# Optimization experiments

Measured on AMD Instinct MI355X. Metric: run time of the kernel, lower is better.

## Reference

```python
import jax, jax.numpy as jnp
import numpy as np

# dims: B batches, N points/batch, S sampled points/batch, M image-projected points/batch,
# V voxels, (H,Wd) range-image size, HID hidden size, NSC scales, NCLS classes
B, N, S, M, V, H, Wd, HID, NSC, NCLS = 2, 120000, 40000, 30000, 100000, 256, 1024, 128, 4, 20


def setup_inputs() -> dict:
    key = jax.random.key(0)
    ks = jax.random.split(key, 24)
    f = jnp.float32
    w = lambda k, shp: (0.02 * jax.random.normal(k, shp, f))
    rows = jax.random.randint(ks[10], (B, M), 0, H, jnp.int32)
    cols = jax.random.randint(ks[11], (B, M), 0, Wd, jnp.int32)
    return {
        "pts_feat_layers": jax.random.normal(ks[0], (NSC, V, HID), f),
        "pts_sample_feat": jax.random.normal(ks[1], (NSC, B * S, HID), f),
        "img_latent_full": jax.random.normal(ks[2], (B, HID, H, Wd), f),
        "img_feat_layers": jax.random.normal(ks[3], (NSC, B * M, HID), f),
        "leaner_W": w(ks[4], (NSC, HID, HID)), "leaner_b": jnp.zeros((NSC, HID), f),
        "fcs1_W": w(ks[5], (NSC, 2 * HID, HID)), "fcs1_b": jnp.zeros((NSC, HID), f),
        "fcs2_W": w(ks[6], (NSC, HID, HID)), "fcs2_b": jnp.zeros((NSC, HID), f),
        "cls_W1": w(ks[7], (NSC * HID, 128)), "cls_b1": jnp.zeros((128,), f),
        "cls_W2": w(ks[8], (128, NCLS)), "cls_b2": jnp.zeros((NCLS,), f),
        "points_img": jnp.stack([rows, cols], axis=-1),              # [B,M,2]
        "point2img_index": jax.random.randint(ks[12], (B, M), 0, N, jnp.int32),
        "sample_index": jax.random.randint(ks[13], (B, S), 0, N, jnp.int32),
        "coors_inv": jax.random.randint(ks[14], (B * N,), 0, V, jnp.int32),
    }


def reference(pts_feat_layers, pts_sample_feat, img_latent_full, img_feat_layers,
              leaner_W, leaner_b, fcs1_W, fcs1_b, fcs2_W, fcs2_b,
              cls_W1, cls_b1, cls_W2, cls_b2,
              points_img, point2img_index, sample_index, coors_inv):
    dt = img_latent_full.dtype
    img_hw = jnp.transpose(img_latent_full, (0, 2, 3, 1))  # [B,H,Wd,HID]
    bar = jnp.arange(B)[:, None]
    # gather image features at projected pixel coords: [B,M,HID]
    img_at_pts = img_hw[bar, points_img[:, :, 0], points_img[:, :, 1]]
    # scatter image features to per-point slots (pts_img_batch_new): [B,N,HID]
    pimg = jax.vmap(lambda idx, v: jnp.zeros((N, HID), dt).at[idx].set(v))(point2img_index, img_at_pts)

    fuse_feats, enc_feats = [], []
    for i in range(NSC):
        # p2img_mapping_spsample: output values depend only on sampled feats + image gather
        sf = pts_sample_feat[i].reshape(B, S, HID)
        sp = jax.vmap(lambda idx, v: jnp.zeros((N, HID), dt).at[idx].set(v))(sample_index, sf)
        sp = sp + pimg  # sample_point_feat == sample_point_feat_f  [B,N,HID]
        # scatter fused point features back into voxel features, then gather per point
        pts_feat = pts_feat_layers[i].at[coors_inv].set(sp.reshape(B * N, HID))
        pts_point = pts_feat[coors_inv].reshape(B, N, HID)
        # p2img_mapping: gather the image-projected points per batch  [B*M,HID]
        pts_g = jnp.take_along_axis(pts_point, point2img_index[:, :, None], axis=1).reshape(B * M, HID)
        fl = jax.nn.relu(pts_g @ leaner_W[i] + leaner_b[i])
        fc = jnp.concatenate([img_feat_layers[i], fl], axis=1) @ fcs1_W[i] + fcs1_b[i]
        fw = jax.nn.sigmoid(fc @ fcs2_W[i] + fcs2_b[i])
        fuse_feats.append(jax.nn.relu(fc * fw))
        enc_feats.append(sp.reshape(B * N, HID))

    seg = jnp.concatenate(fuse_feats, axis=1)                       # [B*M, NSC*HID]
    img_seg_logits = jax.nn.relu(seg @ cls_W1 + cls_b1) @ cls_W2 + cls_b2  # [B*M, NCLS]
    output_3d = jnp.concatenate(enc_feats, axis=1)                  # [B*N, NSC*HID]
    return img_seg_logits, output_3d
```

## Files before the change

kernel.cpp:

```cpp
#include <hip/hip_runtime.h>
#include <hip/hip_bf16.h>
#include <math.h>

#define B_    2
#define N_    120000
#define S_    40000
#define M_    30000
#define V_    100000
#define H_    256
#define WD_   1024
#define HID_  128
#define NSC_  4
#define NCLS_ 20
#define BM_   60000
#define BS_   80000
#define BN_   240000

typedef __attribute__((ext_vector_type(8))) short bfrag8;
typedef __attribute__((ext_vector_type(4))) float facc4;
typedef __attribute__((ext_vector_type(4))) unsigned short usvec4;

__device__ __forceinline__ unsigned short f2bf(float f){
  unsigned u = __builtin_bit_cast(unsigned, f);
  u += 0x7fffu + ((u >> 16) & 1u);
  return (unsigned short)(u >> 16);
}
__device__ __forceinline__ float bf2f(unsigned short s){
  return __builtin_bit_cast(float, ((unsigned)s) << 16);
}

__global__ __launch_bounds__(256) void k_front(
    const float* __restrict__ img, const int* __restrict__ ptsimg,
    unsigned short* __restrict__ iap,
    const int* __restrict__ p2i, const int* __restrict__ si,
    const int* __restrict__ ci,
    int* __restrict__ win_p, int* __restrict__ win_s, int* __restrict__ win_c,
    const float* __restrict__ lW, const float* __restrict__ f1W,
    const float* __restrict__ f2W, const float* __restrict__ c1W,
    const float* __restrict__ c2W,
    unsigned short* __restrict__ lwT, unsigned short* __restrict__ f1T,
    unsigned short* __restrict__ f2T, unsigned short* __restrict__ c1T,
    unsigned short* __restrict__ c2T){
  int bid = blockIdx.x;
  if (bid < 938){
    int t = bid * 256 + threadIdx.x;
    if (t < BM_) atomicMax(&win_p[(t / M_) * N_ + p2i[t]], t);
    if (t < BS_) atomicMax(&win_s[(t / S_) * N_ + si[t]], t);
    if (t < BN_) atomicMax(&win_c[ci[t]], t);
    return;
  }
  if (bid < 2228){
    int t = (bid - 938) * 256 + threadIdx.x;
    if (t < 65536){
      int i = t >> 14, r = t & 16383, n = r >> 7, k = r & 127;
      lwT[i * 16384 + n * 128 + k] = f2bf(lW[i * 16384 + k * 128 + n]);
    } else if (t < 196608){
      int e = t - 65536;
      int i = e >> 15, r = e & 32767, n = r >> 8, k = r & 255;
      f1T[i * 32768 + n * 256 + k] = f2bf(f1W[i * 32768 + k * 128 + n]);
    } else if (t < 262144){
      int e = t - 196608;
      int i = e >> 14, r = e & 16383, n = r >> 7, k = r & 127;
      f2T[i * 16384 + n * 128 + k] = f2bf(f2W[i * 16384 + k * 128 + n]);
    } else if (t < 327680){
      int e = t - 262144;
      int n = e >> 9, k = e & 511;
      c1T[n * 512 + k] = f2bf(c1W[k * 128 + n]);
    } else if (t < 330240){
      int e = t - 327680;
      int n = e >> 7, k = e & 127;
      c2T[n * 128 + k] = f2bf(c2W[k * NCLS_ + n]);
    }
    return;
  }
  {
    int t = (bid - 2228) * 256 + threadIdx.x;
    int r0 = t >> 5, h4 = (t & 31) * 4;
    const size_t st = (size_t)H_ * WD_;
    #pragma unroll
    for (int half = 0; half < 2; half++){
      int row = r0 + half * 30000;
      int r = ptsimg[row * 2 + 0];
      int c = ptsimg[row * 2 + 1];
      const float* base = img + (((size_t)half * HID_ + h4) * H_ + r) * WD_ + c;
      float v0 = base[0], v1 = base[st], v2 = base[2 * st], v3 = base[3 * st];
      usvec4 o = {f2bf(v0), f2bf(v1), f2bf(v2), f2bf(v3)};
      *(usvec4*)(iap + (size_t)row * HID_ + h4) = o;
    }
    return;
  }
}

__global__ __launch_bounds__(256) void k_o3d(const float* __restrict__ samp,
    const int* __restrict__ win_s, const int* __restrict__ win_p,
    const unsigned short* __restrict__ iap, float* __restrict__ o3d){
  const facc4 zero = {0.f, 0.f, 0.f, 0.f};
  int t = blockIdx.x * 256 + threadIdx.x;
  int jg = t >> 5, q = t & 31;
  int j0 = jg << 2;
  int sjv[4], pjv[4];
  #pragma unroll
  for (int jj = 0; jj < 4; jj++){ sjv[jj] = win_s[j0 + jj]; pjv[jj] = win_p[j0 + jj]; }
  facc4 iv[4];
  #pragma unroll
  for (int jj = 0; jj < 4; jj++){
    int p = pjv[jj] < 0 ? 0 : pjv[jj];
    usvec4 u = *(const usvec4*)(iap + (size_t)p * HID_ + q * 4);
    facc4 v = {bf2f(u.x), bf2f(u.y), bf2f(u.z), bf2f(u.w)};
    iv[jj] = pjv[jj] >= 0 ? v : zero;
  }
  #pragma unroll
  for (int i = 0; i < NSC_; i++){
    #pragma unroll
    for (int jj = 0; jj < 4; jj++){
      int s = sjv[jj] < 0 ? 0 : sjv[jj];
      facc4 sv = *(const facc4*)(samp + ((size_t)i * BS_ + s) * HID_ + q * 4);
      facc4 v = iv[jj] + (sjv[jj] >= 0 ? sv : zero);
      __builtin_nontemporal_store(v,
          (facc4*)(o3d + (size_t)(j0 + jj) * (NSC_ * HID_) + i * HID_ + q * 4));
    }
  }
}

__global__ __launch_bounds__(256, 3) void k_scales(
    const float* __restrict__ samp, const unsigned short* __restrict__ iap,
    const int* __restrict__ win_p, const int* __restrict__ win_s,
    const int* __restrict__ win_c, const int* __restrict__ p2i,
    const int* __restrict__ ci, const float* __restrict__ imgf,
    const unsigned short* __restrict__ lwT, const float* __restrict__ lb,
    const unsigned short* __restrict__ f1T, const float* __restrict__ f1b,
    const unsigned short* __restrict__ f2T, const float* __restrict__ f2b,
    unsigned short* __restrict__ seg){
  __shared__ char lds[49152];
  char* actL = lds + 32768;
  const int i  = blockIdx.x & 3;
  const int rb = blockIdx.x >> 2;
  const int lane = threadIdx.x & 63, wv = threadIdx.x >> 6;
  const int rl = lane & 15, kg = lane >> 4;
  const int rowBase = rb * 64 + wv * 16;
  const int row = rowBase + rl;
  const bool rv = row < BM_;
  const int lr = wv * 16 + rl;

  {
    const char* src = (const char*)(lwT + (size_t)i * 16384);
    for (int c = threadIdx.x; c < 2048; c += 256){
      int byte = c << 4; int n = byte >> 8;
      *(bfrag8*)(lds + (byte ^ ((n & 7) << 4))) = *(const bfrag8*)(src + byte);
    }
  }
  bfrag8 afr[4];
  {
    int g = 0;
    if (rv){ int b = row >= M_; g = win_c[ci[b * N_ + p2i[row]]]; }
    int sj = rv ? win_s[g] : -1;
    int pj = rv ? win_p[g] : -1;
    const float* sp = samp + ((size_t)i * BS_ + (sj < 0 ? 0 : sj)) * HID_;
    const unsigned short* pp = iap + (size_t)(pj < 0 ? 0 : pj) * HID_;
    #pragma unroll
    for (int kc = 0; kc < 4; kc++){
      int k0 = kc * 32 + kg * 8;
      facc4 s0 = {0,0,0,0}, s1 = {0,0,0,0};
      if (sj >= 0){ s0 = *(const facc4*)(sp + k0); s1 = *(const facc4*)(sp + k0 + 4); }
      float g0=0,g1=0,g2=0,g3=0,g4=0,g5=0,g6=0,g7=0;
      if (pj >= 0){
        usvec4 u0 = *(const usvec4*)(pp + k0);
        usvec4 u1 = *(const usvec4*)(pp + k0 + 4);
        g0=bf2f(u0.x); g1=bf2f(u0.y); g2=bf2f(u0.z); g3=bf2f(u0.w);
        g4=bf2f(u1.x); g5=bf2f(u1.y); g6=bf2f(u1.z); g7=bf2f(u1.w);
      }
      bfrag8 a;
      a[0]=(short)f2bf(s0.x+g0); a[1]=(short)f2bf(s0.y+g1);
      a[2]=(short)f2bf(s0.z+g2); a[3]=(short)f2bf(s0.w+g3);
      a[4]=(short)f2bf(s1.x+g4); a[5]=(short)f2bf(s1.y+g5);
      a[6]=(short)f2bf(s1.z+g6); a[7]=(short)f2bf(s1.w+g7);
      afr[kc] = a;
    }
  }
  __syncthreads();
  facc4 accL[8];
  #pragma unroll
  for (int ct = 0; ct < 8; ct++) accL[ct] = (facc4){0.f,0.f,0.f,0.f};
  #pragma unroll
  for (int kc = 0; kc < 4; kc++){
    int k0 = kc * 32 + kg * 8;
    #pragma unroll
    for (int ct = 0; ct < 8; ct++){
      int col = ct * 16 + rl;
      int byte = (col << 8) + (k0 << 1);
      bfrag8 b = *(const bfrag8*)(lds + (byte ^ ((col & 7) << 4)));
      accL[ct] = __builtin_amdgcn_mfma_f32_16x16x32_bf16(afr[kc], b, accL[ct], 0, 0, 0);
    }
  }
  __syncthreads();
  {
    const float* bias = lb + i * HID_;
    #pragma unroll
    for (int ct = 0; ct < 8; ct++){
      int col = ct * 16 + rl;
      float bv = bias[col];
      #pragma unroll
      for (int r = 0; r < 4; r++){
        int ar = wv * 16 + kg * 4 + r;
        float v = accL[ct][r] + bv; v = v > 0.f ? v : 0.f;
        int byte = ar * 256 + col * 2;
        *(unsigned short*)(actL + (byte ^ ((ar & 7) << 4))) = f2bf(v);
      }
    }
    const char* src = (const char*)(f1T + (size_t)i * 32768);
    for (int c = threadIdx.x; c < 2048; c += 256){
      int n = c >> 4, off = (c & 15) << 4;
      *(bfrag8*)(lds + ((n * 256 + off) ^ ((n & 7) << 4))) =
          *(const bfrag8*)(src + (size_t)n * 512 + off);
    }
  }
  __syncthreads();
  facc4 accF[8];
  #pragma unroll
  for (int ct = 0; ct < 8; ct++) accF[ct] = (facc4){0.f,0.f,0.f,0.f};
  {
    const float* a1 = imgf + ((size_t)i * BM_ + (rv ? row : 0)) * HID_;
    #pragma unroll
    for (int kc = 0; kc < 4; kc++){
      int kk = kc * 32 + kg * 8;
      bfrag8 a = (bfrag8){0,0,0,0,0,0,0,0};
      if (rv){
        facc4 s0 = *(const facc4*)(a1 + kk);
        facc4 s1 = *(const facc4*)(a1 + kk + 4);
        a[0]=(short)f2bf(s0.x); a[1]=(short)f2bf(s0.y); a[2]=(short)f2bf(s0.z); a[3]=(short)f2bf(s0.w);
        a[4]=(short)f2bf(s1.x); a[5]=(short)f2bf(s1.y); a[6]=(short)f2bf(s1.z); a[7]=(short)f2bf(s1.w);
      }
      #pragma unroll
      for (int ct = 0; ct < 8; ct++){
        int col = ct * 16 + rl;
        int byte = (col << 8) + (kk << 1);
        bfrag8 b = *(const bfrag8*)(lds + (byte ^ ((col & 7) << 4)));
        accF[ct] = __builtin_amdgcn_mfma_f32_16x16x32_bf16(a, b, accF[ct], 0, 0, 0);
      }
    }
  }
  __syncthreads();
  {
    const char* src = (const char*)(f1T + (size_t)i * 32768) + 256;
    for (int c = threadIdx.x; c < 2048; c += 256){
      int n = c >> 4, off = (c & 15) << 4;
      *(bfrag8*)(lds + ((n * 256 + off) ^ ((n & 7) << 4))) =
          *(const bfrag8*)(src + (size_t)n * 512 + off);
    }
  }
  __syncthreads();
  #pragma unroll
  for (int kc = 0; kc < 4; kc++){
    int kl = kc * 32 + kg * 8;
    int byteA = lr * 256 + kl * 2;
    bfrag8 a = *(const bfrag8*)(actL + (byteA ^ ((lr & 7) << 4)));
    #pragma unroll
    for (int ct = 0; ct < 8; ct++){
      int col = ct * 16 + rl;
      int byte = (col << 8) + (kl << 1);
      bfrag8 b = *(const bfrag8*)(lds + (byte ^ ((col & 7) << 4)));
      accF[ct] = __builtin_amdgcn_mfma_f32_16x16x32_bf16(a, b, accF[ct], 0, 0, 0);
    }
  }
  __syncthreads();
  {
    const float* bias = f1b + i * HID_;
    #pragma unroll
    for (int ct = 0; ct < 8; ct++){
      int col = ct * 16 + rl;
      float bv = bias[col];
      #pragma unroll
      for (int r = 0; r < 4; r++){
        int ar = wv * 16 + kg * 4 + r;
        float v = accF[ct][r] + bv;
        accF[ct][r] = v;
        int byte = ar * 256 + col * 2;
        *(unsigned short*)(actL + (byte ^ ((ar & 7) << 4))) = f2bf(v);
      }
    }
    const char* src = (const char*)(f2T + (size_t)i * 16384);
    for (int c = threadIdx.x; c < 2048; c += 256){
      int byte = c << 4; int n = byte >> 8;
      *(bfrag8*)(lds + (byte ^ ((n & 7) << 4))) = *(const bfrag8*)(src + byte);
    }
  }
  __syncthreads();
  facc4 accT[8];
  #pragma unroll
  for (int ct = 0; ct < 8; ct++) accT[ct] = (facc4){0.f,0.f,0.f,0.f};
  #pragma unroll
  for (int kc = 0; kc < 4; kc++){
    int kk = kc * 32 + kg * 8;
    int byteA = lr * 256 + kk * 2;
    bfrag8 a = *(const bfrag8*)(actL + (byteA ^ ((lr & 7) << 4)));
    #pragma unroll
    for (int ct = 0; ct < 8; ct++){
      int col = ct * 16 + rl;
      int byte = (col << 8) + (kk << 1);
      bfrag8 b = *(const bfrag8*)(lds + (byte ^ ((col & 7) << 4)));
      accT[ct] = __builtin_amdgcn_mfma_f32_16x16x32_bf16(a, b, accT[ct], 0, 0, 0);
    }
  }
  {
    const float* bias2 = f2b + i * HID_;
    #pragma unroll
    for (int ct = 0; ct < 8; ct++){
      int col = ct * 16 + rl;
      float bv2 = bias2[col];
      #pragma unroll
      for (int r = 0; r < 4; r++){
        int orow = rowBase + kg * 4 + r;
        if (orow < BM_){
          float tv = accT[ct][r] + bv2;
          float fw = 1.f / (1.f + expf(-tv));
          float u = accF[ct][r] * fw;
          u = u > 0.f ? u : 0.f;
          seg[(size_t)orow * (NSC_ * HID_) + i * HID_ + col] = f2bf(u);
        }
      }
    }
  }
}

__global__ __launch_bounds__(256, 3) void k_cls(const unsigned short* __restrict__ seg,
    const unsigned short* __restrict__ c1T, const float* __restrict__ c1b,
    const unsigned short* __restrict__ c2T, const float* __restrict__ c2b,
    float* __restrict__ logits){
  __shared__ char lds[49152];
  char* actL = lds + 32768;
  const int lane = threadIdx.x & 63, wv = threadIdx.x >> 6;
  const int rl = lane & 15, kg = lane >> 4;
  const int rowBase = blockIdx.x * 64 + wv * 16;
  const int row = rowBase + rl;
  const bool rv = row < BM_;
  const unsigned short* ar = seg + (size_t)(rv ? row : 0) * 512;
  facc4 acc[8];
  #pragma unroll
  for (int ct = 0; ct < 8; ct++) acc[ct] = (facc4){0.f,0.f,0.f,0.f};
  for (int ph = 0; ph < 4; ph++){
    if (ph) __syncthreads();
    for (int c = threadIdx.x; c < 2048; c += 256){
      int n = c >> 4, off = (c & 15) << 4;
      *(bfrag8*)(lds + ((n * 256 + off) ^ ((n & 7) << 4))) =
          *(const bfrag8*)((const char*)c1T + (size_t)n * 1024 + ph * 256 + off);
    }
    __syncthreads();
    #pragma unroll
    for (int kc = 0; kc < 4; kc++){
      int kl = kc * 32 + kg * 8;
      bfrag8 a = (bfrag8){0,0,0,0,0,0,0,0};
      if (rv) a = *(const bfrag8*)(ar + ph * 128 + kl);
      #pragma unroll
      for (int ct = 0; ct < 8; ct++){
        int col = ct * 16 + rl;
        int byte = (col << 8) + (kl << 1);
        bfrag8 b = *(const bfrag8*)(lds + (byte ^ ((col & 7) << 4)));
        acc[ct] = __builtin_amdgcn_mfma_f32_16x16x32_bf16(a, b, acc[ct], 0, 0, 0);
      }
    }
  }
  __syncthreads();
  #pragma unroll
  for (int ct = 0; ct < 8; ct++){
    int col = ct * 16 + rl;
    float bv = c1b[col];
    #pragma unroll
    for (int r = 0; r < 4; r++){
      int arr = wv * 16 + kg * 4 + r;
      float v = acc[ct][r] + bv; v = v > 0.f ? v : 0.f;
      int byte = arr * 256 + col * 2;
      *(unsigned short*)(actL + (byte ^ ((arr & 7) << 4))) = f2bf(v);
    }
  }
  for (int c = threadIdx.x; c < 320; c += 256)
    *(bfrag8*)(lds + (c << 4)) = *(const bfrag8*)((const char*)c2T + (c << 4));
  __syncthreads();
  {
    int t = threadIdx.x;
    int lrd = t >> 2, n0 = (t & 3) * 5;
    int orow = blockIdx.x * 64 + lrd;
    if (orow < BM_){
      float accD[5];
      #pragma unroll
      for (int q = 0; q < 5; q++) accD[q] = c2b[n0 + q];
      #pragma unroll
      for (int k8 = 0; k8 < 16; k8++){
        int byteA = lrd * 256 + (k8 << 4);
        bfrag8 hv = *(const bfrag8*)(actL + (byteA ^ ((lrd & 7) << 4)));
        #pragma unroll
        for (int q = 0; q < 5; q++){
          bfrag8 w8 = *(const bfrag8*)(lds + (n0 + q) * 256 + (k8 << 4));
          #pragma unroll
          for (int e = 0; e < 8; e++)
            accD[q] += bf2f((unsigned short)hv[e]) * bf2f((unsigned short)w8[e]);
        }
      }
      #pragma unroll
      for (int q = 0; q < 5; q++)
        logits[(size_t)orow * NCLS_ + n0 + q] = accD[q];
    }
  }
}

extern "C" void kernel_launch(void* const* d_in, const int* in_sizes, int n_in,
                              void* d_out, int out_size, void* d_ws, size_t ws_size,
                              hipStream_t stream){
  const float* samp = (const float*)d_in[1];
  const float* img  = (const float*)d_in[2];
  const float* imgf = (const float*)d_in[3];
  const float* lW   = (const float*)d_in[4];
  const float* lb   = (const float*)d_in[5];
  const float* f1W  = (const float*)d_in[6];
  const float* f1b  = (const float*)d_in[7];
  const float* f2W  = (const float*)d_in[8];
  const float* f2b  = (const float*)d_in[9];
  const float* c1W  = (const float*)d_in[10];
  const float* c1b  = (const float*)d_in[11];
  const float* c2W  = (const float*)d_in[12];
  const float* c2b  = (const float*)d_in[13];
  const int* ptsimg = (const int*)d_in[14];
  const int* p2i    = (const int*)d_in[15];
  const int* si     = (const int*)d_in[16];
  const int* ci     = (const int*)d_in[17];

  char* ws = (char*)d_ws;
  int*   win_p = (int*)(ws + 0);
  int*   win_s = (int*)(ws + 960000);
  int*   win_c = (int*)(ws + 1920000);
  unsigned short* iap = (unsigned short*)(ws + 2320128);
  unsigned short* seg = (unsigned short*)(ws + 17680384);
  unsigned short* lwT = (unsigned short*)(ws + 79120512);
  unsigned short* f1T = lwT + 65536;
  unsigned short* f2T = f1T + 131072;
  unsigned short* c1T = f2T + 65536;
  unsigned short* c2T = c1T + 65536;

  float* logits = (float*)d_out;
  float* o3d    = (float*)d_out + (size_t)BM_ * NCLS_;

  (void)hipMemsetAsync(ws, 0xFF, 2320000, stream);
  k_front  <<<5978,  256, 0, stream>>>(img, ptsimg, iap, p2i, si, ci,
                                       win_p, win_s, win_c,
                                       lW, f1W, f2W, c1W, c2W,
                                       lwT, f1T, f2T, c1T, c2T);
  k_o3d    <<<7500,  256, 0, stream>>>(samp, win_s, win_p, iap, o3d);
  k_scales <<<3752,  256, 0, stream>>>(samp, iap, win_p, win_s, win_c, p2i, ci,
                                       imgf, lwT, lb, f1T, f1b, f2T, f2b, seg);
  k_cls    <<<938,   256, 0, stream>>>(seg, c1T, c1b, c2T, c2b, logits);
}
```

Baseline: 466.1 us.

## Enlarge k_scales blocks to 128 rows and widen per-thread image gather

k_scales now runs 512-thread blocks covering 128 rows with 64KB of LDS. Each staged weight tile is therefore reused across twice as many rows, which cuts global weight reads and staging passes per row. The image-feature gather in k_front now assigns 4 threads per row, each reading 32 channel values and writing 16-byte bf16 stores, so the grid shrinks. The larger LDS footprint and block size may lower occupancy, and the gather has fewer threads in flight to hide strided-load latency.

```diff
diff --git a/kernel.cpp b/kernel.cpp
--- a/kernel.cpp
+++ b/kernel.cpp
@@ -75,17 +75,24 @@
   }
   {
     int t = (bid - 2228) * 256 + threadIdx.x;
-    int r0 = t >> 5, h4 = (t & 31) * 4;
+    int row = t >> 2;
+    if (row >= BM_) return;
+    int h0 = (t & 3) * 32;
+    int b = row >= M_;
+    int r = ptsimg[row * 2 + 0];
+    int c = ptsimg[row * 2 + 1];
+    const float* base = img + (((size_t)b * HID_ + h0) * H_ + r) * WD_ + c;
     const size_t st = (size_t)H_ * WD_;
-    #pragma unroll
-    for (int half = 0; half < 2; half++){
-      int row = r0 + half * 30000;
-      int r = ptsimg[row * 2 + 0];
-      int c = ptsimg[row * 2 + 1];
-      const float* base = img + (((size_t)half * HID_ + h4) * H_ + r) * WD_ + c;
-      float v0 = base[0], v1 = base[st], v2 = base[2 * st], v3 = base[3 * st];
-      usvec4 o = {f2bf(v0), f2bf(v1), f2bf(v2), f2bf(v3)};
-      *(usvec4*)(iap + (size_t)row * HID_ + h4) = o;
+    unsigned short* dst = iap + (size_t)row * HID_ + h0;
+    #pragma unroll
+    for (int g = 0; g < 4; g++){
+      float v[8];
+      #pragma unroll
+      for (int e = 0; e < 8; e++) v[e] = base[(size_t)(g * 8 + e) * st];
+      bfrag8 o;
+      #pragma unroll
+      for (int e = 0; e < 8; e++) o[e] = (short)f2bf(v[e]);
+      *(bfrag8*)(dst + g * 8) = o;
     }
     return;
   }
@@ -122,7 +129,7 @@
   }
 }
 
-__global__ __launch_bounds__(256, 3) void k_scales(
+__global__ __launch_bounds__(512, 4) void k_scales(
     const float* __restrict__ samp, const unsigned short* __restrict__ iap,
     const int* __restrict__ win_p, const int* __restrict__ win_s,
     const int* __restrict__ win_c, const int* __restrict__ p2i,
@@ -131,20 +138,21 @@
     const unsigned short* __restrict__ f1T, const float* __restrict__ f1b,
     const unsigned short* __restrict__ f2T, const float* __restrict__ f2b,
     unsigned short* __restrict__ seg){
-  __shared__ char lds[49152];
+  __shared__ char lds[65536];
   char* actL = lds + 32768;
   const int i  = blockIdx.x & 3;
   const int rb = blockIdx.x >> 2;
-  const int lane = threadIdx.x & 63, wv = threadIdx.x >> 6;
+  const int tid = threadIdx.x;
+  const int lane = tid & 63, wv = tid >> 6;
   const int rl = lane & 15, kg = lane >> 4;
-  const int rowBase = rb * 64 + wv * 16;
+  const int rowBase = rb * 128 + wv * 16;
   const int row = rowBase + rl;
   const bool rv = row < BM_;
   const int lr = wv * 16 + rl;
 
   {
     const char* src = (const char*)(lwT + (size_t)i * 16384);
-    for (int c = threadIdx.x; c < 2048; c += 256){
+    for (int c = tid; c < 2048; c += 512){
       int byte = c << 4; int n = byte >> 8;
       *(bfrag8*)(lds + (byte ^ ((n & 7) << 4))) = *(const bfrag8*)(src + byte);
     }
@@ -208,7 +216,7 @@
       }
     }
     const char* src = (const char*)(f1T + (size_t)i * 32768);
-    for (int c = threadIdx.x; c < 2048; c += 256){
+    for (int c = tid; c < 2048; c += 512){
       int n = c >> 4, off = (c & 15) << 4;
       *(bfrag8*)(lds + ((n * 256 + off) ^ ((n & 7) << 4))) =
           *(const bfrag8*)(src + (size_t)n * 512 + off);
@@ -242,7 +250,7 @@
   __syncthreads();
   {
     const char* src = (const char*)(f1T + (size_t)i * 32768) + 256;
-    for (int c = threadIdx.x; c < 2048; c += 256){
+    for (int c = tid; c < 2048; c += 512){
       int n = c >> 4, off = (c & 15) << 4;
       *(bfrag8*)(lds + ((n * 256 + off) ^ ((n & 7) << 4))) =
           *(const bfrag8*)(src + (size_t)n * 512 + off);
@@ -279,7 +287,7 @@
       }
     }
     const char* src = (const char*)(f2T + (size_t)i * 16384);
-    for (int c = threadIdx.x; c < 2048; c += 256){
+    for (int c = tid; c < 2048; c += 512){
       int byte = c << 4; int n = byte >> 8;
       *(bfrag8*)(lds + (byte ^ ((n & 7) << 4))) = *(const bfrag8*)(src + byte);
     }
@@ -439,12 +447,12 @@
   float* o3d    = (float*)d_out + (size_t)BM_ * NCLS_;
 
   (void)hipMemsetAsync(ws, 0xFF, 2320000, stream);
-  k_front  <<<5978,  256, 0, stream>>>(img, ptsimg, iap, p2i, si, ci,
+  k_front  <<<3166,  256, 0, stream>>>(img, ptsimg, iap, p2i, si, ci,
                                        win_p, win_s, win_c,
                                        lW, f1W, f2W, c1W, c2W,
                                        lwT, f1T, f2T, c1T, c2T);
   k_o3d    <<<7500,  256, 0, stream>>>(samp, win_s, win_p, iap, o3d);
-  k_scales <<<3752,  256, 0, stream>>>(samp, iap, win_p, win_s, win_c, p2i, ci,
+  k_scales <<<1876,  512, 0, stream>>>(samp, iap, win_p, win_s, win_c, p2i, ci,
                                        imgf, lwT, lb, f1T, f1b, f2T, f2b, seg);
   k_cls    <<<938,   256, 0, stream>>>(seg, c1T, c1b, c2T, c2b, logits);
 }
```

New measurement: 481.2 us. 1.03x slower.

## Split fused per-scale MLP kernel into three persistent-tile GEMM kernels

Applied to the files above, without the earlier changes.

Breaks the single k_scales kernel, which ran leaner, fcs1 and fcs2 back to back with LDS weight reloads and many barriers, into three kernels: k_leaner, k_fcs1 and k_fcs2g. Each block now loads its weight tile into LDS once and reuses it across four 64-row tiles, and fcs1/fcs2 split the output columns in halves to shrink LDS per block. The cost is extra global round-trips for bf16 intermediates (fl and fc, about 15 MB each) and two more kernel launches. Occupancy is also raised to 4 blocks per CU.

```diff
diff --git a/kernel.cpp b/kernel.cpp
--- a/kernel.cpp
+++ b/kernel.cpp
@@ -122,44 +122,51 @@
   }
 }
 
-__global__ __launch_bounds__(256, 3) void k_scales(
+__global__ __launch_bounds__(256, 4) void k_leaner(
     const float* __restrict__ samp, const unsigned short* __restrict__ iap,
     const int* __restrict__ win_p, const int* __restrict__ win_s,
     const int* __restrict__ win_c, const int* __restrict__ p2i,
-    const int* __restrict__ ci, const float* __restrict__ imgf,
+    const int* __restrict__ ci,
     const unsigned short* __restrict__ lwT, const float* __restrict__ lb,
-    const unsigned short* __restrict__ f1T, const float* __restrict__ f1b,
-    const unsigned short* __restrict__ f2T, const float* __restrict__ f2b,
-    unsigned short* __restrict__ seg){
-  __shared__ char lds[49152];
-  char* actL = lds + 32768;
-  const int i  = blockIdx.x & 3;
-  const int rb = blockIdx.x >> 2;
-  const int lane = threadIdx.x & 63, wv = threadIdx.x >> 6;
-  const int rl = lane & 15, kg = lane >> 4;
-  const int rowBase = rb * 64 + wv * 16;
-  const int row = rowBase + rl;
-  const bool rv = row < BM_;
-  const int lr = wv * 16 + rl;
-
+    unsigned short* __restrict__ fl){
+  __shared__ char lds[32768];
+  const int i = blockIdx.x & 3, bis = blockIdx.x >> 2;
+  const int tid = threadIdx.x;
+  const int lane = tid & 63, wv = tid >> 6;
+  const int rl = lane & 15, kg = lane >> 4, kgo = kg * 8;
   {
     const char* src = (const char*)(lwT + (size_t)i * 16384);
-    for (int c = threadIdx.x; c < 2048; c += 256){
+    for (int c = tid; c < 2048; c += 256){
       int byte = c << 4; int n = byte >> 8;
       *(bfrag8*)(lds + (byte ^ ((n & 7) << 4))) = *(const bfrag8*)(src + byte);
     }
   }
-  bfrag8 afr[4];
-  {
-    int g = 0;
-    if (rv){ int b = row >= M_; g = win_c[ci[b * N_ + p2i[row]]]; }
-    int sj = rv ? win_s[g] : -1;
-    int pj = rv ? win_p[g] : -1;
+  int sjv[4], pjv[4];
+  #pragma unroll
+  for (int t = 0; t < 4; t++){
+    int row = (bis * 4 + t) * 64 + wv * 16 + rl;
+    int sj = -1, pj = -1;
+    if (row < BM_){
+      int b = row >= M_;
+      int g = win_c[ci[b * N_ + p2i[row]]];
+      sj = win_s[g]; pj = win_p[g];
+    }
+    sjv[t] = sj; pjv[t] = pj;
+  }
+  __syncthreads();
+  float bv[8];
+  #pragma unroll
+  for (int ct = 0; ct < 8; ct++) bv[ct] = lb[i * HID_ + ct * 16 + rl];
+  #pragma unroll 1
+  for (int t = 0; t < 4; t++){
+    int rowBase = (bis * 4 + t) * 64 + wv * 16;
+    int sj = sjv[t], pj = pjv[t];
     const float* sp = samp + ((size_t)i * BS_ + (sj < 0 ? 0 : sj)) * HID_;
     const unsigned short* pp = iap + (size_t)(pj < 0 ? 0 : pj) * HID_;
+    bfrag8 afr[4];
     #pragma unroll
     for (int kc = 0; kc < 4; kc++){
-      int k0 = kc * 32 + kg * 8;
+      int k0 = kc * 32 + kgo;
       facc4 s0 = {0,0,0,0}, s1 = {0,0,0,0};
       if (sj >= 0){ s0 = *(const facc4*)(sp + k0); s1 = *(const facc4*)(sp + k0 + 4); }
       float g0=0,g1=0,g2=0,g3=0,g4=0,g5=0,g6=0,g7=0;
@@ -176,144 +183,154 @@
       a[6]=(short)f2bf(s1.z+g6); a[7]=(short)f2bf(s1.w+g7);
       afr[kc] = a;
     }
-  }
-  __syncthreads();
-  facc4 accL[8];
-  #pragma unroll
-  for (int ct = 0; ct < 8; ct++) accL[ct] = (facc4){0.f,0.f,0.f,0.f};
-  #pragma unroll
-  for (int kc = 0; kc < 4; kc++){
-    int k0 = kc * 32 + kg * 8;
-    #pragma unroll
-    for (int ct = 0; ct < 8; ct++){
-      int col = ct * 16 + rl;
-      int byte = (col << 8) + (k0 << 1);
-      bfrag8 b = *(const bfrag8*)(lds + (byte ^ ((col & 7) << 4)));
-      accL[ct] = __builtin_amdgcn_mfma_f32_16x16x32_bf16(afr[kc], b, accL[ct], 0, 0, 0);
-    }
-  }
-  __syncthreads();
-  {
-    const float* bias = lb + i * HID_;
-    #pragma unroll
-    for (int ct = 0; ct < 8; ct++){
-      int col = ct * 16 + rl;
-      float bv = bias[col];
-      #pragma unroll
-      for (int r = 0; r < 4; r++){
-        int ar = wv * 16 + kg * 4 + r;
-        float v = accL[ct][r] + bv; v = v > 0.f ? v : 0.f;
-        int byte = ar * 256 + col * 2;
-        *(unsigned short*)(actL + (byte ^ ((ar & 7) << 4))) = f2bf(v);
-      }
-    }
-    const char* src = (const char*)(f1T + (size_t)i * 32768);
-    for (int c = threadIdx.x; c < 2048; c += 256){
-      int n = c >> 4, off = (c & 15) << 4;
-      *(bfrag8*)(lds + ((n * 256 + off) ^ ((n & 7) << 4))) =
-          *(const bfrag8*)(src + (size_t)n * 512 + off);
-    }
-  }
-  __syncthreads();
-  facc4 accF[8];
-  #pragma unroll
-  for (int ct = 0; ct < 8; ct++) accF[ct] = (facc4){0.f,0.f,0.f,0.f};
-  {
-    const float* a1 = imgf + ((size_t)i * BM_ + (rv ? row : 0)) * HID_;
+    facc4 acc[8];
+    #pragma unroll
+    for (int ct = 0; ct < 8; ct++) acc[ct] = (facc4){0.f,0.f,0.f,0.f};
     #pragma unroll
     for (int kc = 0; kc < 4; kc++){
-      int kk = kc * 32 + kg * 8;
-      bfrag8 a = (bfrag8){0,0,0,0,0,0,0,0};
-      if (rv){
-        facc4 s0 = *(const facc4*)(a1 + kk);
-        facc4 s1 = *(const facc4*)(a1 + kk + 4);
-        a[0]=(short)f2bf(s0.x); a[1]=(short)f2bf(s0.y); a[2]=(short)f2bf(s0.z); a[3]=(short)f2bf(s0.w);
-        a[4]=(short)f2bf(s1.x); a[5]=(short)f2bf(s1.y); a[6]=(short)f2bf(s1.z); a[7]=(short)f2bf(s1.w);
-      }
+      int k0 = kc * 32 + kgo;
       #pragma unroll
       for (int ct = 0; ct < 8; ct++){
         int col = ct * 16 + rl;
-        int byte = (col << 8) + (kk << 1);
+        int byte = (col << 8) + (k0 << 1);
         bfrag8 b = *(const bfrag8*)(lds + (byte ^ ((col & 7) << 4)));
-        accF[ct] = __builtin_amdgcn_mfma_f32_16x16x32_bf16(a, b, accF[ct], 0, 0, 0);
-      }
-    }
-  }
-  __syncthreads();
-  {
-    const char* src = (const char*)(f1T + (size_t)i * 32768) + 256;
-    for (int c = threadIdx.x; c < 2048; c += 256){
-      int n = c >> 4, off = (c & 15) << 4;
-      *(bfrag8*)(lds + ((n * 256 + off) ^ ((n & 7) << 4))) =
-          *(const bfrag8*)(src + (size_t)n * 512 + off);
-    }
-  }
-  __syncthreads();
-  #pragma unroll
-  for (int kc = 0; kc < 4; kc++){
-    int kl = kc * 32 + kg * 8;
-    int byteA = lr * 256 + kl * 2;
-    bfrag8 a = *(const bfrag8*)(actL + (byteA ^ ((lr & 7) << 4)));
+        acc[ct] = __builtin_amdgcn_mfma_f32_16x16x32_bf16(afr[kc], b, acc[ct], 0, 0, 0);
+      }
+    }
     #pragma unroll
     for (int ct = 0; ct < 8; ct++){
-      int col = ct * 16 + rl;
-      int byte = (col << 8) + (kl << 1);
-      bfrag8 b = *(const bfrag8*)(lds + (byte ^ ((col & 7) << 4)));
-      accF[ct] = __builtin_amdgcn_mfma_f32_16x16x32_bf16(a, b, accF[ct], 0, 0, 0);
-    }
-  }
-  __syncthreads();
-  {
-    const float* bias = f1b + i * HID_;
-    #pragma unroll
-    for (int ct = 0; ct < 8; ct++){
-      int col = ct * 16 + rl;
-      float bv = bias[col];
-      #pragma unroll
-      for (int r = 0; r < 4; r++){
-        int ar = wv * 16 + kg * 4 + r;
-        float v = accF[ct][r] + bv;
-        accF[ct][r] = v;
-        int byte = ar * 256 + col * 2;
-        *(unsigned short*)(actL + (byte ^ ((ar & 7) << 4))) = f2bf(v);
-      }
-    }
-    const char* src = (const char*)(f2T + (size_t)i * 16384);
-    for (int c = threadIdx.x; c < 2048; c += 256){
-      int byte = c << 4; int n = byte >> 8;
-      *(bfrag8*)(lds + (byte ^ ((n & 7) << 4))) = *(const bfrag8*)(src + byte);
-    }
-  }
-  __syncthreads();
-  facc4 accT[8];
-  #pragma unroll
-  for (int ct = 0; ct < 8; ct++) accT[ct] = (facc4){0.f,0.f,0.f,0.f};
-  #pragma unroll
-  for (int kc = 0; kc < 4; kc++){
-    int kk = kc * 32 + kg * 8;
-    int byteA = lr * 256 + kk * 2;
-    bfrag8 a = *(const bfrag8*)(actL + (byteA ^ ((lr & 7) << 4)));
-    #pragma unroll
-    for (int ct = 0; ct < 8; ct++){
-      int col = ct * 16 + rl;
-      int byte = (col << 8) + (kk << 1);
-      bfrag8 b = *(const bfrag8*)(lds + (byte ^ ((col & 7) << 4)));
-      accT[ct] = __builtin_amdgcn_mfma_f32_16x16x32_bf16(a, b, accT[ct], 0, 0, 0);
-    }
-  }
-  {
-    const float* bias2 = f2b + i * HID_;
-    #pragma unroll
-    for (int ct = 0; ct < 8; ct++){
-      int col = ct * 16 + rl;
-      float bv2 = bias2[col];
       #pragma unroll
       for (int r = 0; r < 4; r++){
         int orow = rowBase + kg * 4 + r;
         if (orow < BM_){
-          float tv = accT[ct][r] + bv2;
+          float v = acc[ct][r] + bv[ct]; v = v > 0.f ? v : 0.f;
+          fl[(size_t)orow * HID_ + ct * 16 + rl] = f2bf(v);
+        }
+      }
+    }
+  }
+}
+
+__global__ __launch_bounds__(256, 4) void k_fcs1(
+    const float* __restrict__ imgf, const unsigned short* __restrict__ fl,
+    const unsigned short* __restrict__ f1T, const float* __restrict__ f1b,
+    unsigned short* __restrict__ fc){
+  __shared__ char lds[32768];
+  const int rem = blockIdx.x & 7, bis = blockIdx.x >> 3;
+  const int i = rem >> 1, h = rem & 1;
+  const int tid = threadIdx.x;
+  const int lane = tid & 63, wv = tid >> 6;
+  const int rl = lane & 15, kg = lane >> 4, kgo = kg * 8;
+  {
+    const char* src = (const char*)(f1T + (size_t)i * 32768) + (size_t)h * 64 * 512;
+    for (int c = tid; c < 2048; c += 256){
+      int nloc = c >> 5, off = (c & 31) << 4;
+      *(bfrag8*)(lds + ((nloc * 512 + off) ^ ((nloc & 7) << 4))) =
+          *(const bfrag8*)(src + (size_t)nloc * 512 + off);
+    }
+  }
+  __syncthreads();
+  float bv[4];
+  #pragma unroll
+  for (int ctl = 0; ctl < 4; ctl++) bv[ctl] = f1b[i * HID_ + h * 64 + ctl * 16 + rl];
+  #pragma unroll 1
+  for (int t = 0; t < 4; t++){
+    int rowBase = (bis * 4 + t) * 64 + wv * 16;
+    int row = rowBase + rl;
+    bool rv = row < BM_;
+    const float* a1 = imgf + ((size_t)i * BM_ + (rv ? row : 0)) * HID_;
+    const unsigned short* a2 = fl + (size_t)(rv ? row : 0) * HID_;
+    bfrag8 afr[8];
+    #pragma unroll
+    for (int kc = 0; kc < 4; kc++){
+      int k0 = kc * 32 + kgo;
+      facc4 s0 = *(const facc4*)(a1 + k0);
+      facc4 s1 = *(const facc4*)(a1 + k0 + 4);
+      bfrag8 a;
+      a[0]=(short)f2bf(s0.x); a[1]=(short)f2bf(s0.y); a[2]=(short)f2bf(s0.z); a[3]=(short)f2bf(s0.w);
+      a[4]=(short)f2bf(s1.x); a[5]=(short)f2bf(s1.y); a[6]=(short)f2bf(s1.z); a[7]=(short)f2bf(s1.w);
+      afr[kc] = a;
+      afr[4 + kc] = *(const bfrag8*)(a2 + k0);
+    }
+    facc4 acc[4];
+    #pragma unroll
+    for (int ctl = 0; ctl < 4; ctl++) acc[ctl] = (facc4){0.f,0.f,0.f,0.f};
+    #pragma unroll
+    for (int kc = 0; kc < 8; kc++){
+      int kb = (kc * 32 + kgo) << 1;
+      #pragma unroll
+      for (int ctl = 0; ctl < 4; ctl++){
+        int nloc = ctl * 16 + rl;
+        bfrag8 b = *(const bfrag8*)(lds + ((nloc * 512 + kb) ^ ((nloc & 7) << 4)));
+        acc[ctl] = __builtin_amdgcn_mfma_f32_16x16x32_bf16(afr[kc], b, acc[ctl], 0, 0, 0);
+      }
+    }
+    #pragma unroll
+    for (int ctl = 0; ctl < 4; ctl++){
+      #pragma unroll
+      for (int r = 0; r < 4; r++){
+        int orow = rowBase + kg * 4 + r;
+        if (orow < BM_)
+          fc[(size_t)orow * HID_ + h * 64 + ctl * 16 + rl] = f2bf(acc[ctl][r] + bv[ctl]);
+      }
+    }
+  }
+}
+
+__global__ __launch_bounds__(256, 4) void k_fcs2g(
+    const unsigned short* __restrict__ fc,
+    const unsigned short* __restrict__ f2T, const float* __restrict__ f2b,
+    unsigned short* __restrict__ seg){
+  __shared__ char lds[16384];
+  const int rem = blockIdx.x & 7, bis = blockIdx.x >> 3;
+  const int i = rem >> 1, h = rem & 1;
+  const int tid = threadIdx.x;
+  const int lane = tid & 63, wv = tid >> 6;
+  const int rl = lane & 15, kg = lane >> 4, kgo = kg * 8;
+  {
+    const char* src = (const char*)(f2T + (size_t)i * 16384) + (size_t)h * 64 * 256;
+    for (int c = tid; c < 1024; c += 256){
+      int nloc = c >> 4, off = (c & 15) << 4;
+      *(bfrag8*)(lds + ((nloc * 256 + off) ^ ((nloc & 7) << 4))) =
+          *(const bfrag8*)(src + (size_t)nloc * 256 + off);
+    }
+  }
+  __syncthreads();
+  float bv[4];
+  #pragma unroll
+  for (int ctl = 0; ctl < 4; ctl++) bv[ctl] = f2b[i * HID_ + h * 64 + ctl * 16 + rl];
+  #pragma unroll 1
+  for (int t = 0; t < 4; t++){
+    int rowBase = (bis * 4 + t) * 64 + wv * 16;
+    int row = rowBase + rl;
+    bool rv = row < BM_;
+    const unsigned short* ar = fc + (size_t)(rv ? row : 0) * HID_;
+    bfrag8 afr[4];
+    #pragma unroll
+    for (int kc = 0; kc < 4; kc++) afr[kc] = *(const bfrag8*)(ar + kc * 32 + kgo);
+    facc4 acc[4];
+    #pragma unroll
+    for (int ctl = 0; ctl < 4; ctl++) acc[ctl] = (facc4){0.f,0.f,0.f,0.f};
+    #pragma unroll
+    for (int kc = 0; kc < 4; kc++){
+      int kb = (kc * 32 + kgo) << 1;
+      #pragma unroll
+      for (int ctl = 0; ctl < 4; ctl++){
+        int nloc = ctl * 16 + rl;
+        bfrag8 b = *(const bfrag8*)(lds + ((nloc * 256 + kb) ^ ((nloc & 7) << 4)));
+        acc[ctl] = __builtin_amdgcn_mfma_f32_16x16x32_bf16(afr[kc], b, acc[ctl], 0, 0, 0);
+      }
+    }
+    #pragma unroll
+    for (int ctl = 0; ctl < 4; ctl++){
+      int col = h * 64 + ctl * 16 + rl;
+      #pragma unroll
+      for (int r = 0; r < 4; r++){
+        int orow = rowBase + kg * 4 + r;
+        if (orow < BM_){
+          float tv = acc[ctl][r] + bv[ctl];
           float fw = 1.f / (1.f + expf(-tv));
-          float u = accF[ct][r] * fw;
+          float u = bf2f(fc[(size_t)orow * HID_ + col]) * fw;
           u = u > 0.f ? u : 0.f;
           seg[(size_t)orow * (NSC_ * HID_) + i * HID_ + col] = f2bf(u);
         }
@@ -429,7 +446,9 @@
   int*   win_c = (int*)(ws + 1920000);
   unsigned short* iap = (unsigned short*)(ws + 2320128);
   unsigned short* seg = (unsigned short*)(ws + 17680384);
-  unsigned short* lwT = (unsigned short*)(ws + 79120512);
+  unsigned short* fl  = (unsigned short*)(ws + 79120512);
+  unsigned short* fc  = (unsigned short*)(ws + 94480640);
+  unsigned short* lwT = (unsigned short*)(ws + 109840768);
   unsigned short* f1T = lwT + 65536;
   unsigned short* f2T = f1T + 131072;
   unsigned short* c1T = f2T + 65536;
@@ -439,12 +458,14 @@
   float* o3d    = (float*)d_out + (size_t)BM_ * NCLS_;
 
   (void)hipMemsetAsync(ws, 0xFF, 2320000, stream);
-  k_front  <<<5978,  256, 0, stream>>>(img, ptsimg, iap, p2i, si, ci,
-                                       win_p, win_s, win_c,
-                                       lW, f1W, f2W, c1W, c2W,
-                                       lwT, f1T, f2T, c1T, c2T);
-  k_o3d    <<<7500,  256, 0, stream>>>(samp, win_s, win_p, iap, o3d);
-  k_scales <<<3752,  256, 0, stream>>>(samp, iap, win_p, win_s, win_c, p2i, ci,
-                                       imgf, lwT, lb, f1T, f1b, f2T, f2b, seg);
-  k_cls    <<<938,   256, 0, stream>>>(seg, c1T, c1b, c2T, c2b, logits);
-}
+  k_front <<<5978, 256, 0, stream>>>(img, ptsimg, iap, p2i, si, ci,
+                                     win_p, win_s, win_c,
+                                     lW, f1W, f2W, c1W, c2W,
+                                     lwT, f1T, f2T, c1T, c2T);
+  k_o3d   <<<7500, 256, 0, stream>>>(samp, win_s, win_p, iap, o3d);
+  k_leaner<<<940,  256, 0, stream>>>(samp, iap, win_p, win_s, win_c, p2i, ci,
+                                     lwT, lb, fl);
+  k_fcs1  <<<1880, 256, 0, stream>>>(imgf, fl, f1T, f1b, fc);
+  k_fcs2g <<<1880, 256, 0, stream>>>(fc, f2T, f2b, seg);
+  k_cls   <<<938,  256, 0, stream>>>(seg, c1T, c1b, c2T, c2b, logits);
+}
```

Result: slower. 640.0 us (+37.3%).
